# Optimization experiments

Hardware: AMD Instinct MI355X
Metric: run time of the kernel (lower is better)

Reference implementation:

```python
import jax, jax.numpy as jnp
import numpy as np

N, E, D_IN, H, L, G = 50000, 800000, 128, 64, 3, 256
EPS_BN = 1e-5


def setup_inputs() -> dict:
    key = jax.random.key(0)
    ks = jax.random.split(key, 8)
    x = jax.random.normal(ks[0], (N, D_IN), dtype=jnp.float32)
    edge_index = jax.random.randint(ks[1], (2, E), 0, N)
    batch = jnp.sort(jax.random.randint(ks[2], (N,), 0, G))
    dims = [D_IN] + [H] * L
    params = {}
    for l in range(L):
        params[f"W{l}"] = jax.random.normal(ks[3 + l], (dims[l], H), jnp.float32) * (1.0 / np.sqrt(dims[l]))
        params[f"b{l}"] = jnp.zeros((H,), jnp.float32)
        params[f"gamma{l}"] = jnp.ones((H,), jnp.float32)
        params[f"beta{l}"] = jnp.zeros((H,), jnp.float32)
    return {"x": x, "edge_index": edge_index, "batch": batch, **params}


def _gcn_forward(x, edge_index, batch, Ws, bs, gammas, betas):
    n = x.shape[0]
    loop = jnp.arange(n)
    # GCNConv adds self-loops, then symmetric D^{-1/2} (A+I) D^{-1/2} normalization
    src = jnp.concatenate([edge_index[0], loop])
    dst = jnp.concatenate([edge_index[1], loop])
    deg = jax.ops.segment_sum(jnp.ones_like(src, jnp.float32), dst, num_segments=n)
    dinv = jax.lax.rsqrt(jnp.maximum(deg, 1.0))  # deg >= 1 thanks to self-loops
    norm = dinv[src] * dinv[dst]  # [E+N]

    zs = []
    z = x
    for W, b, g, be in zip(Ws, bs, gammas, betas):
        h = z @ W  # transform first, then aggregate (PyG GCNConv)
        agg = jax.ops.segment_sum(h[src] * norm[:, None], dst, num_segments=n) + b
        z = jax.nn.relu(agg)
        mu = z.mean(axis=0)
        var = z.var(axis=0)  # biased, as in BatchNorm training mode
        z = (z - mu) * jax.lax.rsqrt(var + EPS_BN) * g + be
        zs.append(z)

    cnt = jnp.maximum(
        jax.ops.segment_sum(jnp.ones((n,), jnp.float32), batch, num_segments=G), 1.0
    )
    gs = [jax.ops.segment_sum(z_, batch, num_segments=G) / cnt[:, None] for z_ in zs]

    zc = jnp.concatenate(zs, axis=1)  # [N, L*H]
    gc = jnp.concatenate(gs, axis=1)  # [G, L*H]

    def l2n(a):
        return a / jnp.maximum(jnp.linalg.norm(a, axis=1, keepdims=True), 1e-12)

    return l2n(zc), l2n(gc)


def reference(x, edge_index, batch, W0, b0, gamma0, beta0, W1, b1, gamma1, beta1, W2, b2, gamma2, beta2):
    return _gcn_forward(
        x, edge_index, batch,
        [W0, W1, W2], [b0, b1, b2],
        [gamma0, gamma1, gamma2], [beta0, beta1, beta2],
    )
```

## Files before the change

kernel.cpp:

```cpp
#include <hip/hip_runtime.h>
#include <hip/hip_fp16.h>
#include <cstdint>
#include <cstddef>

#define N_NODES 50000
#define N_EDGES 800000
#define DIM_IN 128
#define H_DIM 64
#define N_GRAPHS 256
#define EPS_BN 1e-5f
#define GEMM0_BLOCKS 782
#define NC 128
#define CHUNK 6250
#define NB 256
#define BUCKET_NODES 196
#define LSS_CAP 4096
#define SMEM_WORDS (DIM_IN * 64)

struct __align__(16) h8 { __half2 a, b, c, d; };
struct __align__(8)  h4 { __half2 a, b; };

__device__ inline void fma4(float4& a, float s, const float4& w) {
    a.x = fmaf(s, w.x, a.x);
    a.y = fmaf(s, w.y, a.y);
    a.z = fmaf(s, w.z, a.z);
    a.w = fmaf(s, w.w, a.w);
}

__device__ inline h4 pack_h4(float4 v) {
    h4 r;
    r.a = __float22half2_rn(make_float2(v.x, v.y));
    r.b = __float22half2_rn(make_float2(v.z, v.w));
    return r;
}


__global__ __launch_bounds__(256) void cnt_gemm0_k(
        const float* __restrict__ X, const float* __restrict__ W,
        __half* __restrict__ hp, const int* __restrict__ dst,
        int* __restrict__ cntM) {
    __shared__ __align__(16) unsigned int smem[SMEM_WORDS];
    if (blockIdx.x < NC) {
        int* cl = (int*)smem;
        if (threadIdx.x < NB) cl[threadIdx.x] = 0;
        __syncthreads();
        int base = blockIdx.x * CHUNK;
        for (int i = threadIdx.x; i < CHUNK; i += 256) {
            int n = dst[base + i];
            atomicAdd(&cl[n / BUCKET_NODES], 1);
        }
        __syncthreads();
        if (threadIdx.x < NB) cntM[blockIdx.x * NB + threadIdx.x] = cl[threadIdx.x];
        return;
    }
    int gb = blockIdx.x - NC;
    float* Wl = (float*)smem;
    for (int i = threadIdx.x * 4; i < DIM_IN * 64; i += 256 * 4)
        *(float4*)&Wl[i] = *(const float4*)&W[i];
    __syncthreads();
    int c4 = (threadIdx.x & 15) * 4;
    int n0 = gb * 64 + (threadIdx.x >> 4) * 4;
    if (n0 >= N_NODES) return;
    const float* zr = X + (size_t)n0 * DIM_IN;
    float4 acc0 = {0,0,0,0}, acc1 = {0,0,0,0}, acc2 = {0,0,0,0}, acc3 = {0,0,0,0};
    #pragma unroll 4
    for (int k = 0; k < DIM_IN; k += 4) {
        float4 w0 = *(float4*)&Wl[(k + 0) * 64 + c4];
        float4 w1 = *(float4*)&Wl[(k + 1) * 64 + c4];
        float4 w2 = *(float4*)&Wl[(k + 2) * 64 + c4];
        float4 w3 = *(float4*)&Wl[(k + 3) * 64 + c4];
        float4 z0 = *(const float4*)&zr[0 * DIM_IN + k];
        float4 z1 = *(const float4*)&zr[1 * DIM_IN + k];
        float4 z2 = *(const float4*)&zr[2 * DIM_IN + k];
        float4 z3 = *(const float4*)&zr[3 * DIM_IN + k];
        fma4(acc0, z0.x, w0); fma4(acc0, z0.y, w1); fma4(acc0, z0.z, w2); fma4(acc0, z0.w, w3);
        fma4(acc1, z1.x, w0); fma4(acc1, z1.y, w1); fma4(acc1, z1.z, w2); fma4(acc1, z1.w, w3);
        fma4(acc2, z2.x, w0); fma4(acc2, z2.y, w1); fma4(acc2, z2.z, w2); fma4(acc2, z2.w, w3);
        fma4(acc3, z3.x, w0); fma4(acc3, z3.y, w1); fma4(acc3, z3.z, w2); fma4(acc3, z3.w, w3);
    }
    *(h4*)&hp[(size_t)(n0 + 0) * 64 + c4] = pack_h4(acc0);
    *(h4*)&hp[(size_t)(n0 + 1) * 64 + c4] = pack_h4(acc1);
    *(h4*)&hp[(size_t)(n0 + 2) * 64 + c4] = pack_h4(acc2);
    *(h4*)&hp[(size_t)(n0 + 3) * 64 + c4] = pack_h4(acc3);
}


__global__ void scanM_k(const int* __restrict__ cntM, int* __restrict__ baseM,
                        int* __restrict__ beb) {
    __shared__ int colsum[NB];
    int w = threadIdx.x;
    int tot = 0;
    for (int c = 0; c < NC; c++) {
        baseM[c * NB + w] = tot;
        tot += cntM[c * NB + w];
    }
    colsum[w] = tot;
    __syncthreads();
    if (w == 0) {
        int run = 0;
        for (int b = 0; b < NB; b++) { beb[b] = run; run += colsum[b]; }
        beb[NB] = run;
    }
}


__global__ __launch_bounds__(256) void scatter_k(
        const int* __restrict__ src, const int* __restrict__ dst,
        const int* __restrict__ baseM, const int* __restrict__ beb,
        unsigned int* __restrict__ ebuf) {
    __shared__ int rk[NB];
    int c = blockIdx.x;
    if (threadIdx.x < NB) rk[threadIdx.x] = 0;
    __syncthreads();
    int base = c * CHUNK;
    for (int i = threadIdx.x; i < CHUNK; i += 256) {
        int n = dst[base + i];
        int s = src[base + i];
        int w = n / BUCKET_NODES;
        int r = atomicAdd(&rk[w], 1);
        ebuf[beb[w] + baseM[c * NB + w] + r] = ((unsigned)n << 16) | (unsigned)s;
    }
}


__global__ __launch_bounds__(256) void fill_k(
        const unsigned int* __restrict__ ebuf, const int* __restrict__ beb,
        int* __restrict__ counts, int* __restrict__ offsets, float* __restrict__ dinv,
        unsigned short* __restrict__ ssrc) {
    int w = blockIdx.x;
    int n0 = w * BUCKET_NODES;
    int nn = min(BUCKET_NODES, N_NODES - n0);
    int eb = beb[w];
    int ec = beb[w + 1] - eb;
    __shared__ int cnt[BUCKET_NODES];
    __shared__ int sc[NB];
    __shared__ unsigned short lssrc[LSS_CAP];
    int t = threadIdx.x;
    if (t < BUCKET_NODES) cnt[t] = 0;
    __syncthreads();
    for (int i = t; i < ec; i += 256) {
        int nl = (int)(ebuf[eb + i] >> 16) - n0;
        atomicAdd(&cnt[nl], 1);
    }
    __syncthreads();
    int cj = (t < nn) ? cnt[t] : 0;
    sc[t] = cj;
    __syncthreads();
    for (int off = 1; off < NB; off <<= 1) {
        int a = (t >= off) ? sc[t - off] : 0;
        __syncthreads();
        sc[t] += a;
        __syncthreads();
    }
    int offj = sc[t] - cj;
    if (t < nn) {
        int n = n0 + t;
        counts[n] = cj;
        offsets[n] = eb + offj;
        dinv[n] = rsqrtf((float)(cj + 1));
        cnt[t] = offj;
    }
    __syncthreads();
    for (int i = t; i < ec; i += 256) {
        unsigned int e = ebuf[eb + i];
        int nl = (int)(e >> 16) - n0;
        int p = atomicAdd(&cnt[nl], 1);
        unsigned short s = (unsigned short)(e & 0xffffu);
        if (p < LSS_CAP) lssrc[p] = s;
        else ssrc[eb + p] = s;
    }
    __syncthreads();
    int lim = min(ec, LSS_CAP);
    for (int i = t; i < lim; i += 256) ssrc[eb + i] = lssrc[i];
}


__global__ __launch_bounds__(256) void gemm_h_k(
        const __half* __restrict__ Z, const float* __restrict__ W,
        const float* __restrict__ scale, const float* __restrict__ shift,
        __half* __restrict__ hp) {
    __shared__ float Wl[H_DIM * 64];
    __shared__ float scl[64], shl[64];
    for (int i = threadIdx.x * 4; i < H_DIM * 64; i += 256 * 4)
        *(float4*)&Wl[i] = *(const float4*)&W[i];
    if (threadIdx.x < 64) { scl[threadIdx.x] = scale[threadIdx.x]; shl[threadIdx.x] = shift[threadIdx.x]; }
    __syncthreads();
    int c4 = (threadIdx.x & 15) * 4;
    int n0 = blockIdx.x * 64 + (threadIdx.x >> 4) * 4;
    if (n0 >= N_NODES) return;
    float4 acc0 = {0,0,0,0}, acc1 = {0,0,0,0}, acc2 = {0,0,0,0}, acc3 = {0,0,0,0};
    #pragma unroll 4
    for (int k = 0; k < H_DIM; k += 4) {
        float4 w0 = *(float4*)&Wl[(k + 0) * 64 + c4];
        float4 w1 = *(float4*)&Wl[(k + 1) * 64 + c4];
        float4 w2 = *(float4*)&Wl[(k + 2) * 64 + c4];
        float4 w3 = *(float4*)&Wl[(k + 3) * 64 + c4];
        float4 s4 = *(float4*)&scl[k];
        float4 f4 = *(float4*)&shl[k];
        #define DO_NODE(ACC, I)                                                        \
        {   h4 r = *(const h4*)&Z[(size_t)(n0 + I) * 64 + k];                          \
            float2 p = __half22float2(r.a), q = __half22float2(r.b);                   \
            float z0 = fmaf(p.x, s4.x, f4.x), z1 = fmaf(p.y, s4.y, f4.y);              \
            float z2 = fmaf(q.x, s4.z, f4.z), z3 = fmaf(q.y, s4.w, f4.w);              \
            fma4(ACC, z0, w0); fma4(ACC, z1, w1); fma4(ACC, z2, w2); fma4(ACC, z3, w3); }
        DO_NODE(acc0, 0) DO_NODE(acc1, 1) DO_NODE(acc2, 2) DO_NODE(acc3, 3)
        #undef DO_NODE
    }
    *(h4*)&hp[(size_t)(n0 + 0) * 64 + c4] = pack_h4(acc0);
    *(h4*)&hp[(size_t)(n0 + 1) * 64 + c4] = pack_h4(acc1);
    *(h4*)&hp[(size_t)(n0 + 2) * 64 + c4] = pack_h4(acc2);
    *(h4*)&hp[(size_t)(n0 + 3) * 64 + c4] = pack_h4(acc3);
}


__global__ __launch_bounds__(256) void aggregate_k(
        const __half* __restrict__ hp, const float* __restrict__ dinv,
        const int* __restrict__ offsets, const int* __restrict__ counts,
        const unsigned short* __restrict__ ssrc, const float* __restrict__ bias,
        __half* __restrict__ zb) {
    int wid = (blockIdx.x * blockDim.x + threadIdx.x) >> 6;
    int lane = threadIdx.x & 63;
    int g = lane >> 3;
    int c8 = (lane & 7) * 8;
    float a0=0,a1=0,a2=0,a3=0,a4=0,a5=0,a6=0,a7=0;
    int s0 = offsets[wid];
    int ce = counts[wid];
    int e = g;
    for (; e + 8 < ce; e += 16) {
        int s1 = ssrc[s0 + e];
        int s2 = ssrc[s0 + e + 8];
        float d1 = dinv[s1], d2 = dinv[s2];
        h8 v1 = *(const h8*)(hp + (size_t)s1 * 64 + c8);
        h8 v2 = *(const h8*)(hp + (size_t)s2 * 64 + c8);
        float2 f0 = __half22float2(v1.a), f1 = __half22float2(v1.b);
        float2 f2 = __half22float2(v1.c), f3 = __half22float2(v1.d);
        float2 g0 = __half22float2(v2.a), g1 = __half22float2(v2.b);
        float2 g2 = __half22float2(v2.c), g3 = __half22float2(v2.d);
        a0 = fmaf(f0.x, d1, a0); a0 = fmaf(g0.x, d2, a0);
        a1 = fmaf(f0.y, d1, a1); a1 = fmaf(g0.y, d2, a1);
        a2 = fmaf(f1.x, d1, a2); a2 = fmaf(g1.x, d2, a2);
        a3 = fmaf(f1.y, d1, a3); a3 = fmaf(g1.y, d2, a3);
        a4 = fmaf(f2.x, d1, a4); a4 = fmaf(g2.x, d2, a4);
        a5 = fmaf(f2.y, d1, a5); a5 = fmaf(g2.y, d2, a5);
        a6 = fmaf(f3.x, d1, a6); a6 = fmaf(g3.x, d2, a6);
        a7 = fmaf(f3.y, d1, a7); a7 = fmaf(g3.y, d2, a7);
    }
    if (e < ce) {
        int s = ssrc[s0 + e];
        float d1 = dinv[s];
        h8 v = *(const h8*)(hp + (size_t)s * 64 + c8);
        float2 f0 = __half22float2(v.a), f1 = __half22float2(v.b);
        float2 f2 = __half22float2(v.c), f3 = __half22float2(v.d);
        a0 = fmaf(f0.x, d1, a0); a1 = fmaf(f0.y, d1, a1);
        a2 = fmaf(f1.x, d1, a2); a3 = fmaf(f1.y, d1, a3);
        a4 = fmaf(f2.x, d1, a4); a5 = fmaf(f2.y, d1, a5);
        a6 = fmaf(f3.x, d1, a6); a7 = fmaf(f3.y, d1, a7);
    }
    #define RED(A) A += __shfl_xor(A, 8); A += __shfl_xor(A, 16); A += __shfl_xor(A, 32);
    RED(a0) RED(a1) RED(a2) RED(a3) RED(a4) RED(a5) RED(a6) RED(a7)
    #undef RED
    if (g == 0) {
        h8 sv = *(const h8*)(hp + (size_t)wid * 64 + c8);
        float2 f0 = __half22float2(sv.a), f1 = __half22float2(sv.b);
        float2 f2 = __half22float2(sv.c), f3 = __half22float2(sv.d);
        float di = dinv[wid];
        float4 b0 = *(const float4*)&bias[c8];
        float4 b1 = *(const float4*)&bias[c8 + 4];
        float o0 = fmaxf(fmaf(fmaf(f0.x, di, a0), di, b0.x), 0.f);
        float o1 = fmaxf(fmaf(fmaf(f0.y, di, a1), di, b0.y), 0.f);
        float o2 = fmaxf(fmaf(fmaf(f1.x, di, a2), di, b0.z), 0.f);
        float o3 = fmaxf(fmaf(fmaf(f1.y, di, a3), di, b0.w), 0.f);
        float o4 = fmaxf(fmaf(fmaf(f2.x, di, a4), di, b1.x), 0.f);
        float o5 = fmaxf(fmaf(fmaf(f2.y, di, a5), di, b1.y), 0.f);
        float o6 = fmaxf(fmaf(fmaf(f3.x, di, a6), di, b1.z), 0.f);
        float o7 = fmaxf(fmaf(fmaf(f3.y, di, a7), di, b1.w), 0.f);
        h8 ov;
        ov.a = __float22half2_rn(make_float2(o0, o1));
        ov.b = __float22half2_rn(make_float2(o2, o3));
        ov.c = __float22half2_rn(make_float2(o4, o5));
        ov.d = __float22half2_rn(make_float2(o6, o7));
        *(h8*)(zb + (size_t)wid * 64 + c8) = ov;
    }
}


__global__ __launch_bounds__(256) void bn_stats_k(const __half* __restrict__ zb,
                                                  float* __restrict__ slots) {
    int slot = threadIdx.x & 7;
    int rp = threadIdx.x >> 3;
    float s[8], q[8];
    #pragma unroll
    for (int j = 0; j < 8; j++) { s[j] = 0.f; q[j] = 0.f; }
    for (int n = blockIdx.x * 32 + rp; n < N_NODES; n += 256 * 32) {
        h8 v = *(const h8*)(zb + (size_t)n * 64 + slot * 8);
        float2 f0 = __half22float2(v.a), f1 = __half22float2(v.b);
        float2 f2 = __half22float2(v.c), f3 = __half22float2(v.d);
        float x0 = f0.x, x1 = f0.y, x2 = f1.x, x3 = f1.y;
        float x4 = f2.x, x5 = f2.y, x6 = f3.x, x7 = f3.y;
        s[0] += x0; q[0] += x0 * x0; s[1] += x1; q[1] += x1 * x1;
        s[2] += x2; q[2] += x2 * x2; s[3] += x3; q[3] += x3 * x3;
        s[4] += x4; q[4] += x4 * x4; s[5] += x5; q[5] += x5 * x5;
        s[6] += x6; q[6] += x6 * x6; s[7] += x7; q[7] += x7 * x7;
    }
    #pragma unroll
    for (int j = 0; j < 8; j++) {
        float a = s[j];
        a += __shfl_xor(a, 8); a += __shfl_xor(a, 16); a += __shfl_xor(a, 32);
        s[j] = a;
        float b = q[j];
        b += __shfl_xor(b, 8); b += __shfl_xor(b, 16); b += __shfl_xor(b, 32);
        q[j] = b;
    }
    __shared__ float rs[4][64], rq[4][64];
    int w = threadIdx.x >> 6;
    if ((threadIdx.x & 63) < 8) {
        #pragma unroll
        for (int j = 0; j < 8; j++) {
            rs[w][slot * 8 + j] = s[j];
            rq[w][slot * 8 + j] = q[j];
        }
    }
    __syncthreads();
    int t = threadIdx.x;
    int rep = (blockIdx.x & 7) * 128;
    if (t < 64)
        atomicAdd(&slots[rep + t], rs[0][t] + rs[1][t] + rs[2][t] + rs[3][t]);
    else if (t < 128) {
        int c = t - 64;
        atomicAdd(&slots[rep + t], rq[0][c] + rq[1][c] + rq[2][c] + rq[3][c]);
    }
}

__global__ void bn_finalize_k(float* __restrict__ slots,
                              const float* __restrict__ gamma, const float* __restrict__ beta,
                              float* __restrict__ scale, float* __restrict__ shift) {
    __shared__ float red[128];
    int c = threadIdx.x;
    float v = 0.f;
    #pragma unroll
    for (int r = 0; r < 8; r++) v += slots[r * 128 + c];
    red[c] = v;
    __syncthreads();
    if (c < 64) {
        float mu = red[c] * (1.0f / N_NODES);
        float var = red[c + 64] * (1.0f / N_NODES) - mu * mu;
        float k = gamma[c] * rsqrtf(var + EPS_BN);
        scale[c] = k;
        shift[c] = beta[c] - mu * k;
    }
    #pragma unroll
    for (int i = 0; i < 8; i++) slots[i * 128 + c] = 0.f;
}


__global__ __launch_bounds__(256) void pool_k(
        const __half* __restrict__ zb0, const __half* __restrict__ zb1,
        const __half* __restrict__ zb2,
        const float* __restrict__ scaleAll, const float* __restrict__ shiftAll,
        const int* __restrict__ batch, float* __restrict__ gc) {
    int g = blockIdx.x;
    int lo = 0, hi = N_NODES;
    while (lo < hi) { int mid = (lo + hi) >> 1; if (batch[mid] < g) lo = mid + 1; else hi = mid; }
    int start = lo;
    hi = N_NODES;
    while (lo < hi) { int mid = (lo + hi) >> 1; if (batch[mid] < g + 1) lo = mid + 1; else hi = mid; }
    int end = lo;

    int slot = threadIdx.x & 7;
    int r = threadIdx.x >> 3;
    const __half* zbs[3] = {zb0, zb1, zb2};
    float acc[3][8];
    #pragma unroll
    for (int l = 0; l < 3; l++)
        #pragma unroll
        for (int j = 0; j < 8; j++) acc[l][j] = 0.f;
    #pragma unroll
    for (int l = 0; l < 3; l++) {
        const __half* z = zbs[l];
        for (int n = start + r; n < end; n += 32) {
            h8 v = *(const h8*)(z + (size_t)n * 64 + slot * 8);
            float2 f0 = __half22float2(v.a), f1 = __half22float2(v.b);
            float2 f2 = __half22float2(v.c), f3 = __half22float2(v.d);
            acc[l][0] += f0.x; acc[l][1] += f0.y; acc[l][2] += f1.x; acc[l][3] += f1.y;
            acc[l][4] += f2.x; acc[l][5] += f2.y; acc[l][6] += f3.x; acc[l][7] += f3.y;
        }
    }
    #pragma unroll
    for (int l = 0; l < 3; l++)
        #pragma unroll
        for (int j = 0; j < 8; j++) {
            float a = acc[l][j];
            a += __shfl_xor(a, 8);
            a += __shfl_xor(a, 16);
            a += __shfl_xor(a, 32);
            acc[l][j] = a;
        }
    __shared__ float red[4][3][64];
    int w = threadIdx.x >> 6;
    if ((threadIdx.x & 63) < 8) {
        #pragma unroll
        for (int l = 0; l < 3; l++)
            #pragma unroll
            for (int j = 0; j < 8; j++)
                red[w][l][slot * 8 + j] = acc[l][j];
    }
    __syncthreads();
    __shared__ float part[4];
    int t = threadIdx.x;
    float m = 0.f;
    if (t < 192) {
        int l = t >> 6, ch = t & 63;
        float s = red[0][l][ch] + red[1][l][ch] + red[2][l][ch] + red[3][l][ch];
        m = (end > start) ? fmaf(scaleAll[t], s / (float)(end - start), shiftAll[t]) : 0.f;
    }
    float q = m * m;
    #pragma unroll
    for (int off = 32; off; off >>= 1) q += __shfl_xor(q, off);
    if ((t & 63) == 0) part[t >> 6] = q;
    __syncthreads();
    float inv = 1.0f / fmaxf(sqrtf(part[0] + part[1] + part[2] + part[3]), 1e-12f);
    if (t < 192) gc[(size_t)g * 192 + t] = m * inv;
}

__global__ __launch_bounds__(256) void l2norm_zc_k(
        const __half* __restrict__ zb0, const __half* __restrict__ zb1,
        const __half* __restrict__ zb2,
        const float* __restrict__ scaleAll, const float* __restrict__ shiftAll,
        float* __restrict__ zc) {
    int wid = (blockIdx.x * blockDim.x + threadIdx.x) >> 6;
    int lane = threadIdx.x & 63;
    float a = fmaf(__half2float(zb0[(size_t)wid * 64 + lane]), scaleAll[lane],       shiftAll[lane]);
    float b = fmaf(__half2float(zb1[(size_t)wid * 64 + lane]), scaleAll[64 + lane],  shiftAll[64 + lane]);
    float c = fmaf(__half2float(zb2[(size_t)wid * 64 + lane]), scaleAll[128 + lane], shiftAll[128 + lane]);
    float s = a * a + b * b + c * c;
    #pragma unroll
    for (int off = 32; off; off >>= 1) s += __shfl_xor(s, off);
    float inv = 1.0f / fmaxf(sqrtf(s), 1e-12f);
    float* row = zc + (size_t)wid * 192;
    row[lane] = a * inv; row[lane + 64] = b * inv; row[lane + 128] = c * inv;
}


extern "C" void kernel_launch(void* const* d_in, const int* in_sizes, int n_in,
                              void* d_out, int out_size, void* d_ws, size_t ws_size,
                              hipStream_t stream) {
    const float* x     = (const float*)d_in[0];
    const int*   ei    = (const int*)d_in[1];
    const int*   batch = (const int*)d_in[2];
    const float* W[3]     = {(const float*)d_in[3],  (const float*)d_in[7],  (const float*)d_in[11]};
    const float* bias[3]  = {(const float*)d_in[4],  (const float*)d_in[8],  (const float*)d_in[12]};
    const float* gamma[3] = {(const float*)d_in[5],  (const float*)d_in[9],  (const float*)d_in[13]};
    const float* beta[3]  = {(const float*)d_in[6],  (const float*)d_in[10], (const float*)d_in[14]};
    const int* src = ei;
    const int* dst = ei + N_EDGES;

    float* out = (float*)d_out;
    float* zc = out;
    float* gc = out + (size_t)N_NODES * 192;

    char* w = (char*)d_ws;
    auto alloc = [&](size_t bytes) -> void* {
        void* p = (void*)w;
        w += (bytes + 255) / 256 * 256;
        return p;
    };
    int*            counts    = (int*)alloc(N_NODES * 4);
    int*            offsets   = (int*)alloc(N_NODES * 4);
    float*          dinv      = (float*)alloc(N_NODES * 4);
    unsigned short* ssrc      = (unsigned short*)alloc(N_EDGES * 2);
    __half*         hp        = (__half*)alloc((size_t)N_NODES * 64 * 2);
    __half*         zb[3];
    zb[0] = (__half*)alloc((size_t)N_NODES * 64 * 2);
    zb[1] = (__half*)alloc((size_t)N_NODES * 64 * 2);
    zb[2] = (__half*)alloc((size_t)N_NODES * 64 * 2);
    float*          slots     = (float*)alloc(8 * 128 * 4);
    float*          scaleAll  = (float*)alloc(192 * 4);
    float*          shiftAll  = (float*)alloc(192 * 4);
    unsigned int* ebuf  = (unsigned int*)zb[1];
    int*          cntM  = (int*)zb[2];
    int*          baseM = (int*)((char*)zb[2] + NC * NB * 4);
    int*          beb   = (int*)((char*)zb[2] + 2 * NC * NB * 4);

    hipMemsetAsync(slots, 0, 8 * 128 * 4, stream);
    cnt_gemm0_k<<<NC + GEMM0_BLOCKS, 256, 0, stream>>>(x, W[0], hp, dst, cntM);
    scanM_k<<<1, NB, 0, stream>>>(cntM, baseM, beb);
    scatter_k<<<NC, 256, 0, stream>>>(src, dst, baseM, beb, ebuf);
    fill_k<<<NB, 256, 0, stream>>>(ebuf, beb, counts, offsets, dinv, ssrc);

    const int aggBlocks = N_NODES / 4;

    for (int l = 0; l < 3; l++) {
        if (l > 0)
            gemm_h_k<<<GEMM0_BLOCKS, 256, 0, stream>>>(zb[l - 1], W[l],
                                                       scaleAll + (l - 1) * 64, shiftAll + (l - 1) * 64,
                                                       hp);
        aggregate_k<<<aggBlocks, 256, 0, stream>>>(hp, dinv, offsets, counts, ssrc,
                                                   bias[l], zb[l]);
        bn_stats_k<<<256, 256, 0, stream>>>(zb[l], slots);
        bn_finalize_k<<<1, 128, 0, stream>>>(slots, gamma[l], beta[l],
                                             scaleAll + l * 64, shiftAll + l * 64);
    }

    pool_k<<<N_GRAPHS, 256, 0, stream>>>(zb[0], zb[1], zb[2], scaleAll, shiftAll, batch, gc);
    l2norm_zc_k<<<N_NODES / 4, 256, 0, stream>>>(zb[0], zb[1], zb[2], scaleAll, shiftAll, zc);
}
```

Baseline: 204.7 us.

## Pre-scale transformed features by dinv and merge pooling with L2 epilogue

The source-side degree normalization is folded into the feature rows before aggregation: the GEMM epilogue multiplies its outputs by dinv, and a new kernel does the same for the layer-0 features. The gather loop then needs no per-edge dinv loads or FMAs, only plain adds. The graph-pooling and node L2-norm kernels are merged into one launch to save a launch gap. In exchange there is an extra read/write pass over the layer-0 features, and the pre-scaled values are rounded to fp16, which changes precision slightly.

Result: faster. 200.5 us (median of 2 runs) (-2.1%).

```diff
diff --git a/kernel.cpp b/kernel.cpp
--- a/kernel.cpp
+++ b/kernel.cpp
@@ -175,10 +175,27 @@
 }
 
 
+__global__ __launch_bounds__(256) void scale_hp_k(__half* __restrict__ hp,
+                                                  const float* __restrict__ dinv) {
+    int idx = blockIdx.x * 256 + threadIdx.x;
+    if (idx >= N_NODES * 8) return;
+    float d = dinv[idx >> 3];
+    h8 v = *(h8*)(hp + (size_t)idx * 8);
+    float2 f0 = __half22float2(v.a), f1 = __half22float2(v.b);
+    float2 f2 = __half22float2(v.c), f3 = __half22float2(v.d);
+    h8 o;
+    o.a = __float22half2_rn(make_float2(f0.x * d, f0.y * d));
+    o.b = __float22half2_rn(make_float2(f1.x * d, f1.y * d));
+    o.c = __float22half2_rn(make_float2(f2.x * d, f2.y * d));
+    o.d = __float22half2_rn(make_float2(f3.x * d, f3.y * d));
+    *(h8*)(hp + (size_t)idx * 8) = o;
+}
+
+
 __global__ __launch_bounds__(256) void gemm_h_k(
         const __half* __restrict__ Z, const float* __restrict__ W,
         const float* __restrict__ scale, const float* __restrict__ shift,
-        __half* __restrict__ hp) {
+        const float* __restrict__ dinv, __half* __restrict__ hp) {
     __shared__ float Wl[H_DIM * 64];
     __shared__ float scl[64], shl[64];
     for (int i = threadIdx.x * 4; i < H_DIM * 64; i += 256 * 4)
@@ -206,6 +223,11 @@
         DO_NODE(acc0, 0) DO_NODE(acc1, 1) DO_NODE(acc2, 2) DO_NODE(acc3, 3)
         #undef DO_NODE
     }
+    float d0 = dinv[n0], d1 = dinv[n0 + 1], d2 = dinv[n0 + 2], d3 = dinv[n0 + 3];
+    acc0.x *= d0; acc0.y *= d0; acc0.z *= d0; acc0.w *= d0;
+    acc1.x *= d1; acc1.y *= d1; acc1.z *= d1; acc1.w *= d1;
+    acc2.x *= d2; acc2.y *= d2; acc2.z *= d2; acc2.w *= d2;
+    acc3.x *= d3; acc3.y *= d3; acc3.z *= d3; acc3.w *= d3;
     *(h4*)&hp[(size_t)(n0 + 0) * 64 + c4] = pack_h4(acc0);
     *(h4*)&hp[(size_t)(n0 + 1) * 64 + c4] = pack_h4(acc1);
     *(h4*)&hp[(size_t)(n0 + 2) * 64 + c4] = pack_h4(acc2);
@@ -229,32 +251,22 @@
     for (; e + 8 < ce; e += 16) {
         int s1 = ssrc[s0 + e];
         int s2 = ssrc[s0 + e + 8];
-        float d1 = dinv[s1], d2 = dinv[s2];
         h8 v1 = *(const h8*)(hp + (size_t)s1 * 64 + c8);
         h8 v2 = *(const h8*)(hp + (size_t)s2 * 64 + c8);
         float2 f0 = __half22float2(v1.a), f1 = __half22float2(v1.b);
         float2 f2 = __half22float2(v1.c), f3 = __half22float2(v1.d);
         float2 g0 = __half22float2(v2.a), g1 = __half22float2(v2.b);
         float2 g2 = __half22float2(v2.c), g3 = __half22float2(v2.d);
-        a0 = fmaf(f0.x, d1, a0); a0 = fmaf(g0.x, d2, a0);
-        a1 = fmaf(f0.y, d1, a1); a1 = fmaf(g0.y, d2, a1);
-        a2 = fmaf(f1.x, d1, a2); a2 = fmaf(g1.x, d2, a2);
-        a3 = fmaf(f1.y, d1, a3); a3 = fmaf(g1.y, d2, a3);
-        a4 = fmaf(f2.x, d1, a4); a4 = fmaf(g2.x, d2, a4);
-        a5 = fmaf(f2.y, d1, a5); a5 = fmaf(g2.y, d2, a5);
-        a6 = fmaf(f3.x, d1, a6); a6 = fmaf(g3.x, d2, a6);
-        a7 = fmaf(f3.y, d1, a7); a7 = fmaf(g3.y, d2, a7);
+        a0 += f0.x + g0.x; a1 += f0.y + g0.y; a2 += f1.x + g1.x; a3 += f1.y + g1.y;
+        a4 += f2.x + g2.x; a5 += f2.y + g2.y; a6 += f3.x + g3.x; a7 += f3.y + g3.y;
     }
     if (e < ce) {
         int s = ssrc[s0 + e];
-        float d1 = dinv[s];
         h8 v = *(const h8*)(hp + (size_t)s * 64 + c8);
         float2 f0 = __half22float2(v.a), f1 = __half22float2(v.b);
         float2 f2 = __half22float2(v.c), f3 = __half22float2(v.d);
-        a0 = fmaf(f0.x, d1, a0); a1 = fmaf(f0.y, d1, a1);
-        a2 = fmaf(f1.x, d1, a2); a3 = fmaf(f1.y, d1, a3);
-        a4 = fmaf(f2.x, d1, a4); a5 = fmaf(f2.y, d1, a5);
-        a6 = fmaf(f3.x, d1, a6); a7 = fmaf(f3.y, d1, a7);
+        a0 += f0.x; a1 += f0.y; a2 += f1.x; a3 += f1.y;
+        a4 += f2.x; a5 += f2.y; a6 += f3.x; a7 += f3.y;
     }
     #define RED(A) A += __shfl_xor(A, 8); A += __shfl_xor(A, 16); A += __shfl_xor(A, 32);
     RED(a0) RED(a1) RED(a2) RED(a3) RED(a4) RED(a5) RED(a6) RED(a7)
@@ -266,14 +278,14 @@
         float di = dinv[wid];
         float4 b0 = *(const float4*)&bias[c8];
         float4 b1 = *(const float4*)&bias[c8 + 4];
-        float o0 = fmaxf(fmaf(fmaf(f0.x, di, a0), di, b0.x), 0.f);
-        float o1 = fmaxf(fmaf(fmaf(f0.y, di, a1), di, b0.y), 0.f);
-        float o2 = fmaxf(fmaf(fmaf(f1.x, di, a2), di, b0.z), 0.f);
-        float o3 = fmaxf(fmaf(fmaf(f1.y, di, a3), di, b0.w), 0.f);
-        float o4 = fmaxf(fmaf(fmaf(f2.x, di, a4), di, b1.x), 0.f);
-        float o5 = fmaxf(fmaf(fmaf(f2.y, di, a5), di, b1.y), 0.f);
-        float o6 = fmaxf(fmaf(fmaf(f3.x, di, a6), di, b1.z), 0.f);
-        float o7 = fmaxf(fmaf(fmaf(f3.y, di, a7), di, b1.w), 0.f);
+        float o0 = fmaxf(fmaf(a0 + f0.x, di, b0.x), 0.f);
+        float o1 = fmaxf(fmaf(a1 + f0.y, di, b0.y), 0.f);
+        float o2 = fmaxf(fmaf(a2 + f1.x, di, b0.z), 0.f);
+        float o3 = fmaxf(fmaf(a3 + f1.y, di, b0.w), 0.f);
+        float o4 = fmaxf(fmaf(a4 + f2.x, di, b1.x), 0.f);
+        float o5 = fmaxf(fmaf(a5 + f2.y, di, b1.y), 0.f);
+        float o6 = fmaxf(fmaf(a6 + f3.x, di, b1.z), 0.f);
+        float o7 = fmaxf(fmaf(a7 + f3.y, di, b1.w), 0.f);
         h8 ov;
         ov.a = __float22half2_rn(make_float2(o0, o1));
         ov.b = __float22half2_rn(make_float2(o2, o3));
@@ -353,81 +365,78 @@
 }
 
 
-__global__ __launch_bounds__(256) void pool_k(
+__global__ __launch_bounds__(256) void epilogue_k(
         const __half* __restrict__ zb0, const __half* __restrict__ zb1,
         const __half* __restrict__ zb2,
         const float* __restrict__ scaleAll, const float* __restrict__ shiftAll,
-        const int* __restrict__ batch, float* __restrict__ gc) {
-    int g = blockIdx.x;
-    int lo = 0, hi = N_NODES;
-    while (lo < hi) { int mid = (lo + hi) >> 1; if (batch[mid] < g) lo = mid + 1; else hi = mid; }
-    int start = lo;
-    hi = N_NODES;
-    while (lo < hi) { int mid = (lo + hi) >> 1; if (batch[mid] < g + 1) lo = mid + 1; else hi = mid; }
-    int end = lo;
-
-    int slot = threadIdx.x & 7;
-    int r = threadIdx.x >> 3;
-    const __half* zbs[3] = {zb0, zb1, zb2};
-    float acc[3][8];
-    #pragma unroll
-    for (int l = 0; l < 3; l++)
-        #pragma unroll
-        for (int j = 0; j < 8; j++) acc[l][j] = 0.f;
-    #pragma unroll
-    for (int l = 0; l < 3; l++) {
-        const __half* z = zbs[l];
-        for (int n = start + r; n < end; n += 32) {
-            h8 v = *(const h8*)(z + (size_t)n * 64 + slot * 8);
-            float2 f0 = __half22float2(v.a), f1 = __half22float2(v.b);
-            float2 f2 = __half22float2(v.c), f3 = __half22float2(v.d);
-            acc[l][0] += f0.x; acc[l][1] += f0.y; acc[l][2] += f1.x; acc[l][3] += f1.y;
-            acc[l][4] += f2.x; acc[l][5] += f2.y; acc[l][6] += f3.x; acc[l][7] += f3.y;
-        }
-    }
-    #pragma unroll
-    for (int l = 0; l < 3; l++)
-        #pragma unroll
-        for (int j = 0; j < 8; j++) {
-            float a = acc[l][j];
-            a += __shfl_xor(a, 8);
-            a += __shfl_xor(a, 16);
-            a += __shfl_xor(a, 32);
-            acc[l][j] = a;
-        }
-    __shared__ float red[4][3][64];
-    int w = threadIdx.x >> 6;
-    if ((threadIdx.x & 63) < 8) {
+        const int* __restrict__ batch, float* __restrict__ gc,
+        float* __restrict__ zc) {
+    if (blockIdx.x < N_GRAPHS) {
+        int g = blockIdx.x;
+        int lo = 0, hi = N_NODES;
+        while (lo < hi) { int mid = (lo + hi) >> 1; if (batch[mid] < g) lo = mid + 1; else hi = mid; }
+        int start = lo;
+        hi = N_NODES;
+        while (lo < hi) { int mid = (lo + hi) >> 1; if (batch[mid] < g + 1) lo = mid + 1; else hi = mid; }
+        int end = lo;
+
+        int slot = threadIdx.x & 7;
+        int r = threadIdx.x >> 3;
+        const __half* zbs[3] = {zb0, zb1, zb2};
+        float acc[3][8];
         #pragma unroll
         for (int l = 0; l < 3; l++)
             #pragma unroll
-            for (int j = 0; j < 8; j++)
-                red[w][l][slot * 8 + j] = acc[l][j];
-    }
-    __syncthreads();
-    __shared__ float part[4];
-    int t = threadIdx.x;
-    float m = 0.f;
-    if (t < 192) {
-        int l = t >> 6, ch = t & 63;
-        float s = red[0][l][ch] + red[1][l][ch] + red[2][l][ch] + red[3][l][ch];
-        m = (end > start) ? fmaf(scaleAll[t], s / (float)(end - start), shiftAll[t]) : 0.f;
-    }
-    float q = m * m;
-    #pragma unroll
-    for (int off = 32; off; off >>= 1) q += __shfl_xor(q, off);
-    if ((t & 63) == 0) part[t >> 6] = q;
-    __syncthreads();
-    float inv = 1.0f / fmaxf(sqrtf(part[0] + part[1] + part[2] + part[3]), 1e-12f);
-    if (t < 192) gc[(size_t)g * 192 + t] = m * inv;
-}
-
-__global__ __launch_bounds__(256) void l2norm_zc_k(
-        const __half* __restrict__ zb0, const __half* __restrict__ zb1,
-        const __half* __restrict__ zb2,
-        const float* __restrict__ scaleAll, const float* __restrict__ shiftAll,
-        float* __restrict__ zc) {
-    int wid = (blockIdx.x * blockDim.x + threadIdx.x) >> 6;
+            for (int j = 0; j < 8; j++) acc[l][j] = 0.f;
+        #pragma unroll
+        for (int l = 0; l < 3; l++) {
+            const __half* z = zbs[l];
+            for (int n = start + r; n < end; n += 32) {
+                h8 v = *(const h8*)(z + (size_t)n * 64 + slot * 8);
+                float2 f0 = __half22float2(v.a), f1 = __half22float2(v.b);
+                float2 f2 = __half22float2(v.c), f3 = __half22float2(v.d);
+                acc[l][0] += f0.x; acc[l][1] += f0.y; acc[l][2] += f1.x; acc[l][3] += f1.y;
+                acc[l][4] += f2.x; acc[l][5] += f2.y; acc[l][6] += f3.x; acc[l][7] += f3.y;
+            }
+        }
+        #pragma unroll
+        for (int l = 0; l < 3; l++)
+            #pragma unroll
+            for (int j = 0; j < 8; j++) {
+                float a = acc[l][j];
+                a += __shfl_xor(a, 8);
+                a += __shfl_xor(a, 16);
+                a += __shfl_xor(a, 32);
+                acc[l][j] = a;
+            }
+        __shared__ float red[4][3][64];
+        int w = threadIdx.x >> 6;
+        if ((threadIdx.x & 63) < 8) {
+            #pragma unroll
+            for (int l = 0; l < 3; l++)
+                #pragma unroll
+                for (int j = 0; j < 8; j++)
+                    red[w][l][slot * 8 + j] = acc[l][j];
+        }
+        __syncthreads();
+        __shared__ float part[4];
+        int t = threadIdx.x;
+        float m = 0.f;
+        if (t < 192) {
+            int l = t >> 6, ch = t & 63;
+            float s = red[0][l][ch] + red[1][l][ch] + red[2][l][ch] + red[3][l][ch];
+            m = (end > start) ? fmaf(scaleAll[t], s / (float)(end - start), shiftAll[t]) : 0.f;
+        }
+        float q = m * m;
+        #pragma unroll
+        for (int off = 32; off; off >>= 1) q += __shfl_xor(q, off);
+        if ((t & 63) == 0) part[t >> 6] = q;
+        __syncthreads();
+        float inv = 1.0f / fmaxf(sqrtf(part[0] + part[1] + part[2] + part[3]), 1e-12f);
+        if (t < 192) gc[(size_t)g * 192 + t] = m * inv;
+        return;
+    }
+    int wid = ((blockIdx.x - N_GRAPHS) * 256 + threadIdx.x) >> 6;
     int lane = threadIdx.x & 63;
     float a = fmaf(__half2float(zb0[(size_t)wid * 64 + lane]), scaleAll[lane],       shiftAll[lane]);
     float b = fmaf(__half2float(zb1[(size_t)wid * 64 + lane]), scaleAll[64 + lane],  shiftAll[64 + lane]);
@@ -486,6 +495,7 @@
     scanM_k<<<1, NB, 0, stream>>>(cntM, baseM, beb);
     scatter_k<<<NC, 256, 0, stream>>>(src, dst, baseM, beb, ebuf);
     fill_k<<<NB, 256, 0, stream>>>(ebuf, beb, counts, offsets, dinv, ssrc);
+    scale_hp_k<<<(N_NODES * 8 + 255) / 256, 256, 0, stream>>>(hp, dinv);
 
     const int aggBlocks = N_NODES / 4;
 
@@ -493,7 +503,7 @@
         if (l > 0)
             gemm_h_k<<<GEMM0_BLOCKS, 256, 0, stream>>>(zb[l - 1], W[l],
                                                        scaleAll + (l - 1) * 64, shiftAll + (l - 1) * 64,
-                                                       hp);
+                                                       dinv, hp);
         aggregate_k<<<aggBlocks, 256, 0, stream>>>(hp, dinv, offsets, counts, ssrc,
                                                    bias[l], zb[l]);
         bn_stats_k<<<256, 256, 0, stream>>>(zb[l], slots);
@@ -501,6 +511,6 @@
                                              scaleAll + l * 64, shiftAll + l * 64);
     }
 
-    pool_k<<<N_GRAPHS, 256, 0, stream>>>(zb[0], zb[1], zb[2], scaleAll, shiftAll, batch, gc);
-    l2norm_zc_k<<<N_NODES / 4, 256, 0, stream>>>(zb[0], zb[1], zb[2], scaleAll, shiftAll, zc);
-}
+    epilogue_k<<<N_GRAPHS + N_NODES / 4, 256, 0, stream>>>(zb[0], zb[1], zb[2],
+                                                           scaleAll, shiftAll, batch, gc, zc);
+}
```
